# Performance work log

Measured on AMD Instinct MI355X. Metric: run time of the kernel, lower is better.

The kernel has to match this reference:

```python
import jax, jax.numpy as jnp
import numpy as np

EPS = 1e-5
KERNELS = [3, 3, 5, 7]  # 2*i+1 for i>=1, first layer k=3


def _conv_relu_bn(x, w, b, gamma, beta, rmean, rvar):
    # x: [B, Cin, S], w: [Cout, Cin, K]
    k = w.shape[-1]
    y = jax.lax.conv_general_dilated(
        x, w, window_strides=(1,), padding=[(k // 2, k // 2)],
        dimension_numbers=("NCW", "OIW", "NCW"))
    y = y + b[None, :, None]
    y = jax.nn.relu(y)
    # BatchNorm1d in inference mode (running stats)
    inv = gamma[None, :, None] / jnp.sqrt(rvar[None, :, None] + EPS)
    return (y - rmean[None, :, None]) * inv + beta[None, :, None]


def setup_inputs() -> dict:
    key = jax.random.key(0)
    ks = jax.random.split(key, 32)
    B, S = 128, 8192
    inp = {"x": jax.random.normal(ks[0], (B, 4, S), dtype=jnp.float32)}
    cin = 4
    for i, k in enumerate(KERNELS):
        inp[f"w{i}"] = jax.random.normal(ks[1 + i], (32, cin, k), dtype=jnp.float32) * 0.1
        inp[f"b{i}"] = jnp.zeros((32,), jnp.float32)
        inp[f"g{i}"] = jnp.ones((32,), jnp.float32)   # BN gamma
        inp[f"bb{i}"] = jnp.zeros((32,), jnp.float32)  # BN beta
        inp[f"rm{i}"] = jnp.zeros((32,), jnp.float32)  # running mean
        inp[f"rv{i}"] = jnp.ones((32,), jnp.float32)   # running var
        cin = 32
    inp["fw1"] = jax.random.normal(ks[10], (16, 32), dtype=jnp.float32) * 0.1
    inp["fb1"] = jnp.zeros((16,), jnp.float32)
    inp["fw2"] = jax.random.normal(ks[11], (1, 16), dtype=jnp.float32) * 0.1
    inp["fb2"] = jnp.zeros((1,), jnp.float32)
    return inp


def reference(x,
              w0, b0, g0, bb0, rm0, rv0,
              w1, b1, g1, bb1, rm1, rv1,
              w2, b2, g2, bb2, rm2, rv2,
              w3, b3, g3, bb3, rm3, rv3,
              fw1, fb1, fw2, fb2):
    x = _conv_relu_bn(x, w0, b0, g0, bb0, rm0, rv0)
    x = _conv_relu_bn(x, w1, b1, g1, bb1, rm1, rv1)
    x = _conv_relu_bn(x, w2, b2, g2, bb2, rm2, rv2)
    x = _conv_relu_bn(x, w3, b3, g3, bb3, rm3, rv3)
    # [B, 32, S] -> [B, S, 32]; the original per-timestep MLP loop is one batched GEMM
    h = jnp.einsum("bcs,hc->bsh", x, fw1) + fb1
    h = jax.nn.relu(h)  # Dropout(0.1) is identity in eval
    out = jnp.einsum("bsh,oh->bso", h, fw2) + fb2
    return out[..., 0]  # squeeze(-1) -> [B, S]
```

## Files before the change

kernel.cpp:

```cpp
#include <hip/hip_runtime.h>

#define SEQ    8192
#define S_TILE 180
#define NROW   198
#define CS     1608
#define NTHR   512
#define NREC   37
#define BN_HALFOFF (NREC*512)

typedef __attribute__((ext_vector_type(8))) _Float16 half8;
typedef __attribute__((ext_vector_type(4))) _Float16 half4v;
typedef __attribute__((ext_vector_type(4))) float    f32x4;

__device__ __forceinline__ int uni(int v){ return __builtin_amdgcn_readfirstlane(v); }

template<int K>
__device__ __forceinline__ float fold_bias(const float* __restrict__ W, int co,
    const float* __restrict__ gp, const float* __restrict__ bbp,
    const float* __restrict__ rmp, const float* __restrict__ rvp)
{
    float acc = 0.f;
#pragma unroll
    for (int ci = 0; ci < 32; ++ci) {
        float sp = gp[ci] * rsqrtf(rvp[ci] + 1e-5f);
        float tp = bbp[ci] - rmp[ci]*sp;
        float wsum = 0.f;
#pragma unroll
        for (int tap = 0; tap < K; ++tap) wsum += W[(co*32 + ci)*K + tap];
        acc += wsum * tp;
    }
    return acc;
}

extern "C" __global__ void prep_kernel(
    const float* w0, const float* w1, const float* w2, const float* w3,
    const float* b0, const float* g0, const float* bb0, const float* rm0, const float* rv0,
    const float* b1, const float* g1, const float* bb1, const float* rm1, const float* rv1,
    const float* b2, const float* g2, const float* bb2, const float* rm2, const float* rv2,
    const float* b3, const float* g3, const float* bb3, const float* rm3, const float* rv3,
    const float* fw1, const float* fb1, _Float16* ws)
{
    const int tid = threadIdx.x;
    const int rec = blockIdx.x;
    if (rec < NREC) {
        if (tid < 64) {
            const int lane = tid;
            const float* W; const float *gp = nullptr, *rvp = nullptr; int CIN, K, r2;
            if      (rec < 6)  { W = w0;  CIN = 4;  K = 3; r2 = rec;      }
            else if (rec < 12) { W = w1;  CIN = 32; K = 3; r2 = rec - 6;  gp = g0; rvp = rv0; }
            else if (rec < 22) { W = w2;  CIN = 32; K = 5; r2 = rec - 12; gp = g1; rvp = rv1; }
            else if (rec < 36) { W = w3;  CIN = 32; K = 7; r2 = rec - 22; gp = g2; rvp = rv2; }
            else               { W = fw1; CIN = 32; K = 1; r2 = 0;        gp = g3; rvp = rv3; }
            int tap = r2 >> 1, mh = r2 & 1;
            int co  = mh*16 + (lane & 15);
            int ci0 = (lane >> 4) * 8;
            half8 h;
#pragma unroll
            for (int j = 0; j < 8; ++j) {
                int ci = ci0 + j;
                float wv = (ci < CIN) ? W[(co*CIN + ci)*K + tap] : 0.0f;
                if (gp) wv *= gp[ci & 31] * rsqrtf(rvp[ci & 31] + 1e-5f);
                h[j] = (_Float16)wv;
            }
            *(half8*)(ws + rec*512 + lane*8) = h;
        }
    } else {
        float* fa = (float*)(ws + BN_HALFOFF);
        if (tid < 128) {
            int l = tid >> 5, co = tid & 31;
            const float *g, *bb, *rm, *rv, *bi;
            if      (l == 0) { g=g0; bb=bb0; rm=rm0; rv=rv0; bi=b0; }
            else if (l == 1) { g=g1; bb=bb1; rm=rm1; rv=rv1; bi=b1; }
            else if (l == 2) { g=g2; bb=bb2; rm=rm2; rv=rv2; bi=b2; }
            else             { g=g3; bb=bb3; rm=rm3; rv=rv3; bi=b3; }
            float s = g[co] * rsqrtf(rv[co] + 1e-5f);
            float t = bb[co] - rm[co]*s;
            float bias = bi[co];
            if      (l == 1) bias += fold_bias<3>(w1, co, g0, bb0, rm0, rv0);
            else if (l == 2) bias += fold_bias<5>(w2, co, g1, bb1, rm1, rv1);
            else if (l == 3) bias += fold_bias<7>(w3, co, g2, bb2, rm2, rv2);
            fa[(l*32 + co)*2 + 0] = bias;
            fa[(l*32 + co)*2 + 1] = -t / s;
        } else if (tid < 144) {
            int hh = tid - 128;
            float acc = fb1[hh];
#pragma unroll
            for (int c = 0; c < 32; ++c) {
                float s3 = g3[c] * rsqrtf(rv3[c] + 1e-5f);
                float t3 = bb3[c] - rm3[c]*s3;
                acc += fw1[hh*32 + c] * t3;
            }
            fa[256 + hh] = acc;
        }
    }
}

template<int K, int DOFF, bool BC0>
__device__ __forceinline__ void conv_layer(
    const _Float16* __restrict__ rec, const float2* __restrict__ bo,
    const _Float16* in, _Float16* outb, int s0, int ntb, int lane)
{
    const int q = lane >> 4, n = lane & 15;
    const _Float16* bbase = in + (BC0 ? 0 : q*CS) + (ntb*16 + n)*8;

    f32x4 acc[3][2];
#pragma unroll
    for (int nt = 0; nt < 3; ++nt)
#pragma unroll
        for (int mh = 0; mh < 2; ++mh) acc[nt][mh] = (f32x4){0.f, 0.f, 0.f, 0.f};

#pragma unroll
    for (int tap = 0; tap < K; ++tap) {
        half8 a0 = *(const half8*)(rec + (tap*2 + 0)*512 + lane*8);
        half8 a1 = *(const half8*)(rec + (tap*2 + 1)*512 + lane*8);
#pragma unroll
        for (int nt = 0; nt < 3; ++nt) {
            half8 bf = *(const half8*)(bbase + nt*128 + tap*8);
            acc[nt][0] = __builtin_amdgcn_mfma_f32_16x16x32_f16(a0, bf, acc[nt][0], 0, 0, 0);
            acc[nt][1] = __builtin_amdgcn_mfma_f32_16x16x32_f16(a1, bf, acc[nt][1], 0, 0, 0);
        }
    }

#pragma unroll
    for (int nt = 0; nt < 3; ++nt) {
        int pos = (ntb + nt)*16 + n;
        bool oob = (unsigned)(s0 + DOFF + pos) >= SEQ;
#pragma unroll
        for (int mh = 0; mh < 2; ++mh) {
            int co0 = mh*16 + q*4;
            half4v hv;
#pragma unroll
            for (int r = 0; r < 4; ++r) {
                float2 p = bo[co0 + r];
                float v = fmaxf(acc[nt][mh][r] + p.x, 0.0f);
                if (oob) v = p.y;
                hv[r] = (_Float16)v;
            }
            int cb = mh*2 + (q >> 1);
            *(half4v*)(outb + cb*CS + pos*8 + (q & 1)*4) = hv;
        }
    }
}

extern "C" __global__ void __launch_bounds__(NTHR, 6)
dnashape_mfma(const float* __restrict__ x, const _Float16* __restrict__ ws,
              const float* __restrict__ fw2, const float* __restrict__ fb2,
              float* __restrict__ out)
{
    __shared__ _Float16 bufA[2][4*CS];
    __shared__ _Float16 bufB[2][4*CS];

    const int tid  = threadIdx.x;
    const int tile = blockIdx.x;
    const int s0   = tile * S_TILE;
    const int b0i  = blockIdx.y * 2;

    const int timg = tid >> 8;
    {
        const float* xb = x + (b0i + timg)*4*SEQ;
        for (int li = (tid & 255); li < NROW; li += 256) {
            int sg = s0 - 7 + li;
            bool ok = (unsigned)sg < SEQ;
            float v0 = ok ? xb[0*SEQ + sg] : 0.f;
            float v1 = ok ? xb[1*SEQ + sg] : 0.f;
            float v2 = ok ? xb[2*SEQ + sg] : 0.f;
            float v3 = ok ? xb[3*SEQ + sg] : 0.f;
            half8 h0 = {(_Float16)v0, (_Float16)v1, (_Float16)v2, (_Float16)v3, 0, 0, 0, 0};
            *(half8*)(&bufB[timg][0*CS + li*8]) = h0;
        }
        const half8 z8 = {0,0,0,0,0,0,0,0};
        int u = tid & 255;
        if (u < 32) *(half8*)(&bufA[timg][(u >> 3)*CS + (192 + (u & 7))*8]) = z8;
    }
    __syncthreads();

    const int lane = tid & 63;
    const int wv   = uni(tid >> 6);
    const int img  = wv >> 2;
    const int ntb  = (wv & 3) * 3;
    const float*  fa = (const float*)(ws + BN_HALFOFF);
    const float2* bo = (const float2*)fa;

    conv_layer<3, -6, true >(ws +  0*512, bo +  0, bufB[img], bufA[img], s0, ntb, lane);
    __syncthreads();
    conv_layer<3, -5, false>(ws +  6*512, bo + 32, bufA[img], bufB[img], s0, ntb, lane);
    __syncthreads();
    conv_layer<5, -3, false>(ws + 12*512, bo + 64, bufB[img], bufA[img], s0, ntb, lane);
    __syncthreads();
    conv_layer<7,  0, false>(ws + 22*512, bo + 96, bufA[img], bufB[img], s0, ntb, lane);
    __syncthreads();

    {
        const int q = lane >> 4, n = lane & 15;
        half8 am = *(const half8*)(ws + 36*512 + lane*8);
        float fb1v[4], fw2v[4];
#pragma unroll
        for (int r = 0; r < 4; ++r) { fb1v[r] = fa[256 + q*4 + r]; fw2v[r] = fw2[q*4 + r]; }
        float fb2v = fb2[0];
        const int b = b0i + img;
#pragma unroll
        for (int nt = 0; nt < 3; ++nt) {
            int pos = (ntb + nt)*16 + n;
            half8 bf = *(const half8*)(&bufB[img][q*CS + pos*8]);
            f32x4 d = {0.f, 0.f, 0.f, 0.f};
            d = __builtin_amdgcn_mfma_f32_16x16x32_f16(am, bf, d, 0, 0, 0);
            float part = 0.f;
#pragma unroll
            for (int r = 0; r < 4; ++r) part += fmaxf(d[r] + fb1v[r], 0.f)*fw2v[r];
            part += __shfl_xor(part, 16, 64);
            part += __shfl_xor(part, 32, 64);
            if (lane < 16) {
                int g = s0 + pos;
                if (pos < S_TILE && g < SEQ) out[b*SEQ + g] = part + fb2v;
            }
        }
    }
}

extern "C" void kernel_launch(void* const* d_in, const int* in_sizes, int n_in,
                              void* d_out, int out_size, void* d_ws, size_t ws_size,
                              hipStream_t stream) {
    const float* p[29];
    for (int i = 0; i < 29; ++i) p[i] = (const float*)d_in[i];
    _Float16* ws = (_Float16*)d_ws;

    prep_kernel<<<dim3(NREC + 1), 144, 0, stream>>>(
        p[1], p[7], p[13], p[19],
        p[2], p[3], p[4], p[5], p[6],
        p[8], p[9], p[10], p[11], p[12],
        p[14], p[15], p[16], p[17], p[18],
        p[20], p[21], p[22], p[23], p[24],
        p[25], p[26], ws);

    dim3 grid((SEQ + S_TILE - 1) / S_TILE, 64);
    dnashape_mfma<<<grid, NTHR, 0, stream>>>(p[0], (const _Float16*)ws,
                                             p[27], p[28], (float*)d_out);
}
```

Measured before the change: 170.8 us.

## Switch conv stack to 32x32x16 MFMA with one image per block

Replaces the 16x16x32 MFMA tiles with 32x32x16 MFMA, repacking activations in LDS as 16-half rows (two channel halves). Layer 0 is folded into a single MFMA by im2col-packing its 3 taps × 4 channels into one K=16 slice. Each block now covers one image with 256 threads and a wider 244-position tile, which reduces halo overhead and improves MFMA efficiency. The trade-off is fewer waves per block, a different occupancy bound (launch bounds 4), and rewritten weight packing in prep.

```diff
diff --git a/kernel.cpp b/kernel.cpp
--- a/kernel.cpp
+++ b/kernel.cpp
@@ -1,16 +1,17 @@
 #include <hip/hip_runtime.h>
 
 #define SEQ    8192
-#define S_TILE 180
-#define NROW   198
-#define CS     1608
-#define NTHR   512
-#define NREC   37
+#define NPOS   256
+#define S_TILE 244
+#define NROWS  264
+#define CSH    (NROWS*16)
+#define NTHR   256
+#define NREC   33
 #define BN_HALFOFF (NREC*512)
 
-typedef __attribute__((ext_vector_type(8))) _Float16 half8;
-typedef __attribute__((ext_vector_type(4))) _Float16 half4v;
-typedef __attribute__((ext_vector_type(4))) float    f32x4;
+typedef __attribute__((ext_vector_type(8)))  _Float16 half8;
+typedef __attribute__((ext_vector_type(4)))  _Float16 half4v;
+typedef __attribute__((ext_vector_type(16))) float    f32x16;
 
 __device__ __forceinline__ int uni(int v){ return __builtin_amdgcn_readfirstlane(v); }
 
@@ -44,23 +45,36 @@
     const int rec = blockIdx.x;
     if (rec < NREC) {
         if (tid < 64) {
-            const int lane = tid;
-            const float* W; const float *gp = nullptr, *rvp = nullptr; int CIN, K, r2;
-            if      (rec < 6)  { W = w0;  CIN = 4;  K = 3; r2 = rec;      }
-            else if (rec < 12) { W = w1;  CIN = 32; K = 3; r2 = rec - 6;  gp = g0; rvp = rv0; }
-            else if (rec < 22) { W = w2;  CIN = 32; K = 5; r2 = rec - 12; gp = g1; rvp = rv1; }
-            else if (rec < 36) { W = w3;  CIN = 32; K = 7; r2 = rec - 22; gp = g2; rvp = rv2; }
-            else               { W = fw1; CIN = 32; K = 1; r2 = 0;        gp = g3; rvp = rv3; }
-            int tap = r2 >> 1, mh = r2 & 1;
-            int co  = mh*16 + (lane & 15);
-            int ci0 = (lane >> 4) * 8;
+            const int lane = tid, co = lane & 31, hi = lane >> 5;
             half8 h;
-#pragma unroll
-            for (int j = 0; j < 8; ++j) {
-                int ci = ci0 + j;
-                float wv = (ci < CIN) ? W[(co*CIN + ci)*K + tap] : 0.0f;
-                if (gp) wv *= gp[ci & 31] * rsqrtf(rvp[ci & 31] + 1e-5f);
-                h[j] = (_Float16)wv;
+            if (rec == 0) {
+#pragma unroll
+                for (int j = 0; j < 8; ++j) {
+                    int k = hi*8 + j;
+                    float wv = 0.f;
+                    if (k < 12) wv = w0[(co*4 + (k & 3))*3 + (k >> 2)];
+                    h[j] = (_Float16)wv;
+                }
+            } else if (rec < 31) {
+                const float* W; const float *gp, *rvp; int K, r2;
+                if      (rec < 7)  { W = w1; K = 3; r2 = rec - 1;  gp = g0; rvp = rv0; }
+                else if (rec < 17) { W = w2; K = 5; r2 = rec - 7;  gp = g1; rvp = rv1; }
+                else               { W = w3; K = 7; r2 = rec - 17; gp = g2; rvp = rv2; }
+                const int tap = r2 >> 1, cib = r2 & 1;
+#pragma unroll
+                for (int j = 0; j < 8; ++j) {
+                    int ci = cib*16 + hi*8 + j;
+                    float s = gp[ci] * rsqrtf(rvp[ci] + 1e-5f);
+                    h[j] = (_Float16)(W[(co*32 + ci)*K + tap] * s);
+                }
+            } else {
+                const int cib = rec - 31;
+#pragma unroll
+                for (int j = 0; j < 8; ++j) {
+                    int ci = cib*16 + hi*8 + j;
+                    float s = g3[ci] * rsqrtf(rv3[ci] + 1e-5f);
+                    h[j] = (_Float16)((co < 16) ? fw1[co*32 + ci]*s : 0.f);
+                }
             }
             *(half8*)(ws + rec*512 + lane*8) = h;
         }
@@ -95,124 +109,164 @@
     }
 }
 
-template<int K, int DOFF, bool BC0>
-__device__ __forceinline__ void conv_layer(
+__device__ __forceinline__ void conv_epi(
+    f32x16* acc, const float2* __restrict__ bo,
+    _Float16* outb, int s0, int doff, int P0, int n, int hi)
+{
+    float2 pv[16];
+#pragma unroll
+    for (int g = 0; g < 4; ++g)
+#pragma unroll
+        for (int i = 0; i < 4; ++i) pv[g*4 + i] = bo[g*8 + 4*hi + i];
+
+#pragma unroll
+    for (int t = 0; t < 2; ++t) {
+        const int pos = P0 + t*32 + n;
+        const bool oob = (unsigned)(s0 + doff + pos) >= SEQ;
+#pragma unroll
+        for (int g = 0; g < 4; ++g) {
+            half4v hv;
+#pragma unroll
+            for (int i = 0; i < 4; ++i) {
+                const float2 p = pv[g*4 + i];
+                const float v = fmaxf(acc[t][g*4 + i] + p.x, 0.f);
+                hv[i] = (_Float16)(oob ? p.y : v);
+            }
+            *(half4v*)(outb + (g >> 1)*CSH + pos*16 + (g & 1)*8 + hi*4) = hv;
+        }
+    }
+}
+
+template<int K, int DOFF>
+__device__ __forceinline__ void conv32(
     const _Float16* __restrict__ rec, const float2* __restrict__ bo,
-    const _Float16* in, _Float16* outb, int s0, int ntb, int lane)
-{
-    const int q = lane >> 4, n = lane & 15;
-    const _Float16* bbase = in + (BC0 ? 0 : q*CS) + (ntb*16 + n)*8;
-
-    f32x4 acc[3][2];
-#pragma unroll
-    for (int nt = 0; nt < 3; ++nt)
-#pragma unroll
-        for (int mh = 0; mh < 2; ++mh) acc[nt][mh] = (f32x4){0.f, 0.f, 0.f, 0.f};
+    const _Float16* in, _Float16* outb, int s0, int P0, int lane)
+{
+    const int n = lane & 31, hi = lane >> 5;
+    const _Float16* bbase = in + (P0 + n)*16 + hi*8;
+
+    f32x16 acc[2];
+#pragma unroll
+    for (int t = 0; t < 2; ++t)
+#pragma unroll
+        for (int i = 0; i < 16; ++i) acc[t][i] = 0.f;
 
 #pragma unroll
     for (int tap = 0; tap < K; ++tap) {
         half8 a0 = *(const half8*)(rec + (tap*2 + 0)*512 + lane*8);
         half8 a1 = *(const half8*)(rec + (tap*2 + 1)*512 + lane*8);
 #pragma unroll
-        for (int nt = 0; nt < 3; ++nt) {
-            half8 bf = *(const half8*)(bbase + nt*128 + tap*8);
-            acc[nt][0] = __builtin_amdgcn_mfma_f32_16x16x32_f16(a0, bf, acc[nt][0], 0, 0, 0);
-            acc[nt][1] = __builtin_amdgcn_mfma_f32_16x16x32_f16(a1, bf, acc[nt][1], 0, 0, 0);
-        }
-    }
-
-#pragma unroll
-    for (int nt = 0; nt < 3; ++nt) {
-        int pos = (ntb + nt)*16 + n;
-        bool oob = (unsigned)(s0 + DOFF + pos) >= SEQ;
-#pragma unroll
-        for (int mh = 0; mh < 2; ++mh) {
-            int co0 = mh*16 + q*4;
-            half4v hv;
-#pragma unroll
-            for (int r = 0; r < 4; ++r) {
-                float2 p = bo[co0 + r];
-                float v = fmaxf(acc[nt][mh][r] + p.x, 0.0f);
-                if (oob) v = p.y;
-                hv[r] = (_Float16)v;
-            }
-            int cb = mh*2 + (q >> 1);
-            *(half4v*)(outb + cb*CS + pos*8 + (q & 1)*4) = hv;
-        }
-    }
-}
-
-extern "C" __global__ void __launch_bounds__(NTHR, 6)
+        for (int t = 0; t < 2; ++t) {
+            half8 b0 = *(const half8*)(bbase + 0*CSH + (t*32 + tap)*16);
+            half8 b1 = *(const half8*)(bbase + 1*CSH + (t*32 + tap)*16);
+            acc[t] = __builtin_amdgcn_mfma_f32_32x32x16_f16(a0, b0, acc[t], 0, 0, 0);
+            acc[t] = __builtin_amdgcn_mfma_f32_32x32x16_f16(a1, b1, acc[t], 0, 0, 0);
+        }
+    }
+    conv_epi(acc, bo, outb, s0, DOFF, P0, n, hi);
+}
+
+__device__ __forceinline__ void conv32L0(
+    const _Float16* __restrict__ rec, const float2* __restrict__ bo,
+    const _Float16* in, _Float16* outb, int s0, int P0, int lane)
+{
+    const int n = lane & 31, hi = lane >> 5;
+    half8 a = *(const half8*)(rec + lane*8);
+    f32x16 acc[2];
+#pragma unroll
+    for (int t = 0; t < 2; ++t)
+#pragma unroll
+        for (int i = 0; i < 16; ++i) acc[t][i] = 0.f;
+#pragma unroll
+    for (int t = 0; t < 2; ++t) {
+        half8 b = *(const half8*)(in + (P0 + t*32 + n)*16 + hi*8);
+        acc[t] = __builtin_amdgcn_mfma_f32_32x32x16_f16(a, b, acc[t], 0, 0, 0);
+    }
+    conv_epi(acc, bo, outb, s0, -6, P0, n, hi);
+}
+
+extern "C" __global__ void __launch_bounds__(NTHR, 4)
 dnashape_mfma(const float* __restrict__ x, const _Float16* __restrict__ ws,
               const float* __restrict__ fw2, const float* __restrict__ fb2,
               float* __restrict__ out)
 {
-    __shared__ _Float16 bufA[2][4*CS];
-    __shared__ _Float16 bufB[2][4*CS];
-
-    const int tid  = threadIdx.x;
-    const int tile = blockIdx.x;
-    const int s0   = tile * S_TILE;
-    const int b0i  = blockIdx.y * 2;
-
-    const int timg = tid >> 8;
+    __shared__ _Float16 bufA[2*CSH] __attribute__((aligned(16)));
+    __shared__ _Float16 bufB[2*CSH] __attribute__((aligned(16)));
+
+    const int tid = threadIdx.x;
+    const int s0  = blockIdx.x * S_TILE;
+    const int b   = blockIdx.y;
+
     {
-        const float* xb = x + (b0i + timg)*4*SEQ;
-        for (int li = (tid & 255); li < NROW; li += 256) {
-            int sg = s0 - 7 + li;
-            bool ok = (unsigned)sg < SEQ;
-            float v0 = ok ? xb[0*SEQ + sg] : 0.f;
-            float v1 = ok ? xb[1*SEQ + sg] : 0.f;
-            float v2 = ok ? xb[2*SEQ + sg] : 0.f;
-            float v3 = ok ? xb[3*SEQ + sg] : 0.f;
-            half8 h0 = {(_Float16)v0, (_Float16)v1, (_Float16)v2, (_Float16)v3, 0, 0, 0, 0};
-            *(half8*)(&bufB[timg][0*CS + li*8]) = h0;
-        }
-        const half8 z8 = {0,0,0,0,0,0,0,0};
-        int u = tid & 255;
-        if (u < 32) *(half8*)(&bufA[timg][(u >> 3)*CS + (192 + (u & 7))*8]) = z8;
+        const float* xb = x + b*4*SEQ;
+        const int r  = tid;
+        const int sb = s0 - 7 + r;
+        _Float16 h[16];
+#pragma unroll
+        for (int tap = 0; tap < 3; ++tap) {
+            const int sg = sb + tap;
+            const bool ok = (unsigned)sg < SEQ;
+#pragma unroll
+            for (int ci = 0; ci < 4; ++ci)
+                h[tap*4 + ci] = (_Float16)(ok ? xb[ci*SEQ + sg] : 0.f);
+        }
+#pragma unroll
+        for (int j = 12; j < 16; ++j) h[j] = (_Float16)0.f;
+        *(half8*)(bufB + r*16)     = *(half8*)(h);
+        *(half8*)(bufB + r*16 + 8) = *(half8*)(h + 8);
+        if (tid < 64) {
+            const half8 z = {0,0,0,0,0,0,0,0};
+            _Float16* base = (tid & 32) ? bufA : bufB;
+            *(half8*)(base + ((tid >> 4) & 1)*CSH + 256*16 + (tid & 15)*8) = z;
+        }
     }
     __syncthreads();
 
     const int lane = tid & 63;
     const int wv   = uni(tid >> 6);
-    const int img  = wv >> 2;
-    const int ntb  = (wv & 3) * 3;
+    const int P0   = wv * 64;
     const float*  fa = (const float*)(ws + BN_HALFOFF);
     const float2* bo = (const float2*)fa;
 
-    conv_layer<3, -6, true >(ws +  0*512, bo +  0, bufB[img], bufA[img], s0, ntb, lane);
-    __syncthreads();
-    conv_layer<3, -5, false>(ws +  6*512, bo + 32, bufA[img], bufB[img], s0, ntb, lane);
-    __syncthreads();
-    conv_layer<5, -3, false>(ws + 12*512, bo + 64, bufB[img], bufA[img], s0, ntb, lane);
-    __syncthreads();
-    conv_layer<7,  0, false>(ws + 22*512, bo + 96, bufA[img], bufB[img], s0, ntb, lane);
+    conv32L0     (ws,           bo,      bufB, bufA, s0, P0, lane);
+    __syncthreads();
+    conv32<3, -5>(ws + 1*512,   bo + 32, bufA, bufB, s0, P0, lane);
+    __syncthreads();
+    conv32<5, -3>(ws + 7*512,   bo + 64, bufB, bufA, s0, P0, lane);
+    __syncthreads();
+    conv32<7,  0>(ws + 17*512,  bo + 96, bufA, bufB, s0, P0, lane);
     __syncthreads();
 
     {
-        const int q = lane >> 4, n = lane & 15;
-        half8 am = *(const half8*)(ws + 36*512 + lane*8);
-        float fb1v[4], fw2v[4];
-#pragma unroll
-        for (int r = 0; r < 4; ++r) { fb1v[r] = fa[256 + q*4 + r]; fw2v[r] = fw2[q*4 + r]; }
-        float fb2v = fb2[0];
-        const int b = b0i + img;
-#pragma unroll
-        for (int nt = 0; nt < 3; ++nt) {
-            int pos = (ntb + nt)*16 + n;
-            half8 bf = *(const half8*)(&bufB[img][q*CS + pos*8]);
-            f32x4 d = {0.f, 0.f, 0.f, 0.f};
-            d = __builtin_amdgcn_mfma_f32_16x16x32_f16(am, bf, d, 0, 0, 0);
+        const int n = lane & 31, hi = lane >> 5;
+        half8 am0 = *(const half8*)(ws + 31*512 + lane*8);
+        half8 am1 = *(const half8*)(ws + 32*512 + lane*8);
+        float fb1v[8], fw2v[8];
+#pragma unroll
+        for (int r = 0; r < 8; ++r) {
+            const int co = (r & 3) + 8*(r >> 2) + 4*hi;
+            fb1v[r] = fa[256 + co];
+            fw2v[r] = fw2[co];
+        }
+        const float fb2v = fb2[0];
+#pragma unroll
+        for (int t = 0; t < 2; ++t) {
+            const int pos = P0 + t*32 + n;
+            half8 bf0 = *(const half8*)(bufB + 0*CSH + pos*16 + hi*8);
+            half8 bf1 = *(const half8*)(bufB + 1*CSH + pos*16 + hi*8);
+            f32x16 d;
+#pragma unroll
+            for (int i = 0; i < 16; ++i) d[i] = 0.f;
+            d = __builtin_amdgcn_mfma_f32_32x32x16_f16(am0, bf0, d, 0, 0, 0);
+            d = __builtin_amdgcn_mfma_f32_32x32x16_f16(am1, bf1, d, 0, 0, 0);
             float part = 0.f;
 #pragma unroll
-            for (int r = 0; r < 4; ++r) part += fmaxf(d[r] + fb1v[r], 0.f)*fw2v[r];
-            part += __shfl_xor(part, 16, 64);
+            for (int r = 0; r < 8; ++r)
+                part += fmaxf(d[r] + fb1v[r], 0.f) * fw2v[r];
             part += __shfl_xor(part, 32, 64);
-            if (lane < 16) {
-                int g = s0 + pos;
-                if (pos < S_TILE && g < SEQ) out[b*SEQ + g] = part + fb2v;
-            }
+            const int gpos = s0 + pos;
+            if (hi == 0 && pos < S_TILE && gpos < SEQ)
+                out[b*SEQ + gpos] = part + fb2v;
         }
     }
 }
@@ -232,7 +286,7 @@
         p[20], p[21], p[22], p[23], p[24],
         p[25], p[26], ws);
 
-    dim3 grid((SEQ + S_TILE - 1) / S_TILE, 64);
+    dim3 grid((SEQ + S_TILE - 1) / S_TILE, 128);
     dnashape_mfma<<<grid, NTHR, 0, stream>>>(p[0], (const _Float16*)ws,
                                              p[27], p[28], (float*)d_out);
 }
```

After: 171.2 us. No clear change (+0.2%).
